# Kernel tuning notes

Measured on AMD Instinct MI355X. Metric: run time of the kernel, lower is better.

The kernel has to match this reference:

```python
import jax, jax.numpy as jnp
import numpy as np

GRID = 4
N_NODES = GRID * GRID
HEADS = 4
HID = 64

def _grid_edges(g=GRID):
    edges = []
    for i in range(g):
        for j in range(g):
            n = i * g + j
            if j + 1 < g:
                edges += [[n, n + 1], [n + 1, n]]
            if i + 1 < g:
                edges += [[n, n + g], [n + g, n]]
    for n in range(g * g):  # PyG GATConv default add_self_loops=True
        edges.append([n, n])
    e = np.asarray(edges, dtype=np.int32).T
    return jnp.asarray(e[0]), jnp.asarray(e[1])  # src (j), dst (i)

SRC, DST = _grid_edges()


def _layernorm(x, g, b, eps=1e-5):
    m = x.mean(-1, keepdims=True)
    v = ((x - m) ** 2).mean(-1, keepdims=True)
    return (x - m) * jax.lax.rsqrt(v + eps) * g + b


def _gat_conv(x, W, a_src, a_dst, bias, concat):
    # x: (B,N,Cin); W: (Cin,H*F); a_src,a_dst: (H,F)
    B, N, _ = x.shape
    H, F = a_src.shape
    xp = (x @ W).reshape(B, N, H, F)
    es = jnp.einsum('bnhf,hf->bnh', xp, a_src)  # alpha_src per node
    ed = jnp.einsum('bnhf,hf->bnh', xp, a_dst)  # alpha_dst per node
    logits = jax.nn.leaky_relu(es[:, SRC] + ed[:, DST], 0.2)  # (B,E,H)
    lt = logits.transpose(1, 0, 2)  # (E,B,H) for segment ops over edges
    mx = jax.ops.segment_max(lt, DST, num_segments=N)
    w = jnp.exp(lt - mx[DST])
    denom = jax.ops.segment_sum(w, DST, num_segments=N)
    alpha = w / denom[DST]  # softmax over incoming edges per dst node
    msg = alpha[..., None] * xp[:, SRC].transpose(1, 0, 2, 3)  # (E,B,H,F)
    out = jax.ops.segment_sum(msg, DST, num_segments=N).transpose(1, 0, 2, 3)  # (B,N,H,F)
    out = out.reshape(B, N, H * F) if concat else out.mean(axis=2)
    return out + bias


def _forward(x, in_w, in_b,
             gat0_w, gat0_asrc, gat0_adst, gat0_b,
             gat1_w, gat1_asrc, gat1_adst, gat1_b,
             gat2_w, gat2_asrc, gat2_adst, gat2_b,
             mlp_w1, mlp_b1, ln1_g, ln1_b,
             mlp_w2, mlp_b2, ln2_g, ln2_b):
    B = x.shape[0]
    # grid->graph: (B,C,H,W) -> (B, N, C)
    nodes = x.transpose(0, 2, 3, 1).reshape(B, N_NODES, -1)
    h = jax.nn.relu(nodes @ in_w + in_b)
    h = _gat_conv(h, gat0_w, gat0_asrc, gat0_adst, gat0_b, concat=True)
    h = jax.nn.relu(h)  # dropout is eval-mode identity
    h = _gat_conv(h, gat1_w, gat1_asrc, gat1_adst, gat1_b, concat=True)
    h = jax.nn.relu(h)
    h = _gat_conv(h, gat2_w, gat2_asrc, gat2_adst, gat2_b, concat=False)
    g = h.mean(axis=1)  # global_mean_pool over the fixed 16-node graph
    y = jax.nn.relu(_layernorm(g @ mlp_w1 + mlp_b1, ln1_g, ln1_b))
    out = jax.nn.relu(_layernorm(y @ mlp_w2 + mlp_b2, ln2_g, ln2_b))
    return out


def setup_inputs() -> dict:
    key = jax.random.key(0)
    ks = jax.random.split(key, 32)
    B, CIN, H, F = 4096, 16, HEADS, HID
    s = 0.1
    d = {
        'x': jax.random.normal(ks[0], (B, CIN, GRID, GRID), jnp.float32),
        'in_w': jax.random.normal(ks[1], (CIN, F)) * s,
        'in_b': jnp.zeros((F,)),
        'gat0_w': jax.random.normal(ks[2], (F, H * F)) * s,
        'gat0_asrc': jax.random.normal(ks[3], (H, F)) * s,
        'gat0_adst': jax.random.normal(ks[4], (H, F)) * s,
        'gat0_b': jnp.zeros((H * F,)),
        'gat1_w': jax.random.normal(ks[5], (H * F, H * F)) * s,
        'gat1_asrc': jax.random.normal(ks[6], (H, F)) * s,
        'gat1_adst': jax.random.normal(ks[7], (H, F)) * s,
        'gat1_b': jnp.zeros((H * F,)),
        'gat2_w': jax.random.normal(ks[8], (H * F, H * F)) * s,
        'gat2_asrc': jax.random.normal(ks[9], (H, F)) * s,
        'gat2_adst': jax.random.normal(ks[10], (H, F)) * s,
        'gat2_b': jnp.zeros((F,)),
        'mlp_w1': jax.random.normal(ks[11], (F, 128)) * s,
        'mlp_b1': jnp.zeros((128,)),
        'ln1_g': jnp.ones((128,)),
        'ln1_b': jnp.zeros((128,)),
        'mlp_w2': jax.random.normal(ks[12], (128, 256)) * s,
        'mlp_b2': jnp.zeros((256,)),
        'ln2_g': jnp.ones((256,)),
        'ln2_b': jnp.zeros((256,)),
    }
    return d


def reference(x, in_w, in_b,
              gat0_w, gat0_asrc, gat0_adst, gat0_b,
              gat1_w, gat1_asrc, gat1_adst, gat1_b,
              gat2_w, gat2_asrc, gat2_adst, gat2_b,
              mlp_w1, mlp_b1, ln1_g, ln1_b,
              mlp_w2, mlp_b2, ln2_g, ln2_b):
    return _forward(x, in_w, in_b,
                    gat0_w, gat0_asrc, gat0_adst, gat0_b,
                    gat1_w, gat1_asrc, gat1_adst, gat1_b,
                    gat2_w, gat2_asrc, gat2_adst, gat2_b,
                    mlp_w1, mlp_b1, ln1_g, ln1_b,
                    mlp_w2, mlp_b2, ln2_g, ln2_b)
```

## Files before the change

kernel.cpp:

```cpp
#include <hip/hip_runtime.h>
#include <math.h>

#define TPB 256
typedef short bfrag __attribute__((ext_vector_type(8)));
typedef float facc4 __attribute__((ext_vector_type(4)));
typedef unsigned int u32;

#define O_INW 0
#define O_G0  2048
#define O_G1  19456
#define O_G2  89088
#define O_W1  158720
#define O_W2  166912

__device__ __forceinline__ short f2bf(float x) {
    u32 u = __float_as_uint(x);
    u32 r = (u + 0x7fffu + ((u >> 16) & 1u)) >> 16;
    return (short)r;
}
__device__ __forceinline__ u32 pk2bf(float lo, float hi) {
    return ((u32)(unsigned short)f2bf(hi) << 16) | (u32)(unsigned short)f2bf(lo);
}

__device__ __forceinline__ int ht_sw(int row, int col) {
    return row * 256 + (col ^ ((row & 7) << 3));
}

__device__ __forceinline__ void pack_frag(const float* __restrict__ W, short* __restrict__ out,
                                          int blk, int NCOL, int TSTR) {
    int u = blk * 256 + threadIdx.x;
    int NT = NCOL >> 4;
    int j = u & 7, l = (u >> 3) & 63, q = u >> 9;
    int nt = q % NT, s = q / NT;
    int k = 32 * s + 8 * (l >> 4) + j;
    int c = 16 * nt + (l & 15);
    out[((s * TSTR + nt) * 64 + l) * 8 + j] = f2bf(W[k * NCOL + c]);
}

__device__ __forceinline__ void pack_fold(const float* __restrict__ W,
                                          const float* __restrict__ as_, const float* __restrict__ ad_,
                                          short* __restrict__ out, int blk, int TSTR) {
    int u = blk * 256 + threadIdx.x;
    int j = u & 7, l = (u >> 3) & 63, s = u >> 9;
    int c = l & 15;
    int k = 32 * s + 8 * (l >> 4) + j;
    float v = 0.f;
    if (c < 8) {
        int h = c >> 1;
        const float* a = (c & 1) ? ad_ : as_;
        for (int f = 0; f < 64; ++f) v += W[k * 256 + h * 64 + f] * a[h * 64 + f];
    }
    out[((s * TSTR + 16) * 64 + l) * 8 + j] = f2bf(v);
}

__device__ __forceinline__ void pack_inw(const float* __restrict__ inw, short* __restrict__ out, int blk) {
    int u = blk * 256 + threadIdx.x;
    int j = u & 7, l = (u >> 3) & 63, nt = u >> 9;
    int k = 8 * (l >> 4) + j;
    out[u] = (k < 16) ? f2bf(inw[k * 64 + 16 * nt + (l & 15)]) : (short)0;
}

__global__ void prep_all(const float* __restrict__ g0w, const float* __restrict__ g1w,
                         const float* __restrict__ g2w, const float* __restrict__ mw1,
                         const float* __restrict__ mw2, const float* __restrict__ inw,
                         const float* __restrict__ g0as, const float* __restrict__ g0ad,
                         const float* __restrict__ g1as, const float* __restrict__ g1ad,
                         const float* __restrict__ g2as, const float* __restrict__ g2ad,
                         short* __restrict__ ws) {
    int blk = blockIdx.x;
    if      (blk < 64)  pack_frag(g0w, ws + O_G0, blk,        256, 17);
    else if (blk < 320) pack_frag(g1w, ws + O_G1, blk - 64,   256, 17);
    else if (blk < 576) pack_frag(g2w, ws + O_G2, blk - 320,  256, 17);
    else if (blk < 608) pack_frag(mw1, ws + O_W1, blk - 576,  128, 8);
    else if (blk < 736) pack_frag(mw2, ws + O_W2, blk - 608,  256, 16);
    else if (blk < 744) pack_inw(inw, ws + O_INW, blk - 736);
    else if (blk < 748) pack_fold(g0w, g0as, g0ad, ws + O_G0, blk - 744, 17);
    else if (blk < 764) pack_fold(g1w, g1as, g1ad, ws + O_G1, blk - 748, 17);
    else                pack_fold(g2w, g2as, g2ad, ws + O_G2, blk - 764, 17);
}

template<int KSTEPS>
__device__ __forceinline__ void gat_core(
    const short* s_htA, const short* s_htB, const short* __restrict__ Wp,
    short* s_alphaM, short* s_xpA, short* s_xpB,
    facc4 agg[2][4]) {

    const int t = threadIdx.x;
    const int w = t >> 6, lane = t & 63, g = lane >> 4, ci = lane & 15;
    const facc4 fz = {0.f, 0.f, 0.f, 0.f};
    const bfrag* Wf = (const bfrag*)Wp;

    facc4 acc[2][4] = {{fz, fz, fz, fz}, {fz, fz, fz, fz}};
    facc4 acce = fz;
#pragma unroll 2
    for (int s = 0; s < KSTEPS; ++s) {
        bfrag a0 = *(const bfrag*)(s_htA + ht_sw(ci, s * 32 + g * 8));
        bfrag a1 = *(const bfrag*)(s_htB + ht_sw(ci, s * 32 + g * 8));
#pragma unroll
        for (int tt = 0; tt < 4; ++tt) {
            bfrag bf = Wf[(s * 17 + 4 * w + tt) * 64 + lane];
            acc[0][tt] = __builtin_amdgcn_mfma_f32_16x16x32_bf16(a0, bf, acc[0][tt], 0, 0, 0);
            acc[1][tt] = __builtin_amdgcn_mfma_f32_16x16x32_bf16(a1, bf, acc[1][tt], 0, 0, 0);
        }
        if (w < 2) {
            bfrag bfold = Wf[(s * 17 + 16) * 64 + lane];
            acce = __builtin_amdgcn_mfma_f32_16x16x32_bf16(w == 0 ? a0 : a1, bfold, acce, 0, 0, 0);
        }
    }

#pragma unroll
    for (int tt = 0; tt < 4; ++tt) {
        int col = 64 * w + 16 * tt + ci;
        *(uint2*)(s_xpA + col * 16 + 4 * g) =
            make_uint2(pk2bf(acc[0][tt][0], acc[0][tt][1]), pk2bf(acc[0][tt][2], acc[0][tt][3]));
        *(uint2*)(s_xpB + col * 16 + 4 * g) =
            make_uint2(pk2bf(acc[1][tt][0], acc[1][tt][1]), pk2bf(acc[1][tt][2], acc[1][tt][3]));
    }
    if (w < 2 && ci < 8) {
        int h = ci >> 1, isD = ci & 1;
#pragma unroll
        for (int r = 0; r < 4; ++r) {
            int idx = (4 * g + r) * 4 + h;
            float* padf = (float*)(s_alphaM + idx * 40 + 32);
            padf[w * 2 + isD] = acce[r];
        }
    }
    __syncthreads();

    if (t < 128) {
        int gr = t >> 6, tl = t & 63, d = tl & 15, h = tl >> 4;
        int ii = d >> 2, jj = d & 3;
        const int go = gr * 2;
        float edv = ((const float*)(s_alphaM + (d * 4 + h) * 40 + 32))[go + 1];
        bool v1 = (jj > 0), v2 = (jj < 3), v3 = (ii > 0), v4 = (ii < 3);
        int s1 = v1 ? d - 1 : d, s2 = v2 ? d + 1 : d;
        int s3 = v3 ? d - 4 : d, s4 = v4 ? d + 4 : d;
        float e0 = ((const float*)(s_alphaM + (d  * 4 + h) * 40 + 32))[go];
        float e1 = ((const float*)(s_alphaM + (s1 * 4 + h) * 40 + 32))[go];
        float e2 = ((const float*)(s_alphaM + (s2 * 4 + h) * 40 + 32))[go];
        float e3 = ((const float*)(s_alphaM + (s3 * 4 + h) * 40 + 32))[go];
        float e4 = ((const float*)(s_alphaM + (s4 * 4 + h) * 40 + 32))[go];
        float l0 = e0 + edv; l0 = (l0 > 0.f) ? l0 : 0.2f * l0;
        float l1 = e1 + edv; l1 = (l1 > 0.f) ? l1 : 0.2f * l1; l1 = v1 ? l1 : -1e30f;
        float l2 = e2 + edv; l2 = (l2 > 0.f) ? l2 : 0.2f * l2; l2 = v2 ? l2 : -1e30f;
        float l3 = e3 + edv; l3 = (l3 > 0.f) ? l3 : 0.2f * l3; l3 = v3 ? l3 : -1e30f;
        float l4 = e4 + edv; l4 = (l4 > 0.f) ? l4 : 0.2f * l4; l4 = v4 ? l4 : -1e30f;
        float mx = fmaxf(fmaxf(fmaxf(l0, l1), fmaxf(l2, l3)), l4);
        float w0 = __expf(l0 - mx), w1 = __expf(l1 - mx), w2 = __expf(l2 - mx);
        float w3 = __expf(l3 - mx), w4 = __expf(l4 - mx);
        float inv = 1.f / (w0 + w1 + w2 + w3 + w4);
        short* base = s_alphaM + (h * 16 + d) * 40 + gr * 16;
        base[s1] = f2bf(w1 * inv);
        base[s2] = f2bf(w2 * inv);
        base[s3] = f2bf(w3 * inv);
        base[s4] = f2bf(w4 * inv);
        base[d]  = f2bf(w0 * inv);
    }
    __syncthreads();

    bfrag araw = *(const bfrag*)(s_alphaM + (w * 16 + ci) * 40 + g * 8);
    const bfrag zf = {};
    bfrag af0 = (g < 2) ? araw : zf;
    bfrag af1 = (g < 2) ? zf : araw;
    const short* xsrc = (g < 2) ? s_xpA : s_xpB;
    const int xoff = (g & 1) * 8;
#pragma unroll
    for (int tt = 0; tt < 4; ++tt) {
        int col = 64 * w + 16 * tt + ci;
        bfrag xf = *(const bfrag*)(xsrc + col * 16 + xoff);
        agg[0][tt] = __builtin_amdgcn_mfma_f32_16x16x32_bf16(af0, xf, fz, 0, 0, 0);
        agg[1][tt] = __builtin_amdgcn_mfma_f32_16x16x32_bf16(af1, xf, fz, 0, 0, 0);
    }
}

__global__ __launch_bounds__(TPB, 4) void gat_fused(
    const float* __restrict__ x,  const float* __restrict__ in_b,
    const short* __restrict__ ws,
    const float* __restrict__ g0_b, const float* __restrict__ g1_b, const float* __restrict__ g2_b,
    const float* __restrict__ b1,   const float* __restrict__ ln1g, const float* __restrict__ ln1b,
    const float* __restrict__ b2,   const float* __restrict__ ln2g, const float* __restrict__ ln2b,
    float* __restrict__ out) {

    __shared__ __align__(16) short s_ht[2][16 * 256];
    __shared__ __align__(16) short s_xpA[256 * 16];
    __shared__ __align__(16) short s_xpB[256 * 16];
    __shared__ __align__(16) short s_alphaM[64 * 40];

    float* s_hsum = (float*)s_ht;
    short* s_gb   = (short*)((char*)s_ht + 2048);
    short* s_y2b  = (short*)((char*)s_ht + 2304);
    float* s_part = (float*)((char*)s_ht + 2816);

    const int b = blockIdx.x, t = threadIdx.x;
    const int w = t >> 6, lane = t & 63, g = lane >> 4, ci = lane & 15;
    const facc4 fz = {0.f, 0.f, 0.f, 0.f};

    {
        int row = t >> 2, q = t & 3;
        *(uint4*)(s_alphaM + row * 40 + q * 8) = make_uint4(0, 0, 0, 0);
    }

    {
        bfrag a0 = {}, a1 = {};
        if (g < 2) {
            float xv0[8], xv1[8];
#pragma unroll
            for (int j = 0; j < 8; ++j) {
                xv0[j] = x[(2 * b)     * 256 + (8 * g + j) * 16 + ci];
                xv1[j] = x[(2 * b + 1) * 256 + (8 * g + j) * 16 + ci];
            }
            u32* ap0 = (u32*)&a0; u32* ap1 = (u32*)&a1;
#pragma unroll
            for (int j = 0; j < 4; ++j) {
                ap0[j] = pk2bf(xv0[2 * j], xv0[2 * j + 1]);
                ap1[j] = pk2bf(xv1[2 * j], xv1[2 * j + 1]);
            }
        }
        bfrag bw = ((const bfrag*)(ws + O_INW))[w * 64 + lane];
        facc4 h0 = __builtin_amdgcn_mfma_f32_16x16x32_bf16(a0, bw, fz, 0, 0, 0);
        facc4 h1 = __builtin_amdgcn_mfma_f32_16x16x32_bf16(a1, bw, fz, 0, 0, 0);
        float ib = in_b[16 * w + ci];
#pragma unroll
        for (int r = 0; r < 4; ++r) {
            s_ht[0][ht_sw(4 * g + r, 16 * w + ci)] = f2bf(fmaxf(h0[r] + ib, 0.f));
            s_ht[1][ht_sw(4 * g + r, 16 * w + ci)] = f2bf(fmaxf(h1[r] + ib, 0.f));
        }
    }
    __syncthreads();

    facc4 agg[2][4];

    gat_core<2>(s_ht[0], s_ht[1], ws + O_G0, s_alphaM, s_xpA, s_xpB, agg);
#pragma unroll
    for (int tt = 0; tt < 4; ++tt) {
        float bb = g0_b[64 * w + 16 * tt + ci];
#pragma unroll
        for (int gr = 0; gr < 2; ++gr)
#pragma unroll
            for (int r = 0; r < 4; ++r)
                s_ht[gr][ht_sw(4 * g + r, 64 * w + 16 * tt + ci)] = f2bf(fmaxf(agg[gr][tt][r] + bb, 0.f));
    }
    __syncthreads();

    gat_core<8>(s_ht[0], s_ht[1], ws + O_G1, s_alphaM, s_xpA, s_xpB, agg);
#pragma unroll
    for (int tt = 0; tt < 4; ++tt) {
        float bb = g1_b[64 * w + 16 * tt + ci];
#pragma unroll
        for (int gr = 0; gr < 2; ++gr)
#pragma unroll
            for (int r = 0; r < 4; ++r)
                s_ht[gr][ht_sw(4 * g + r, 64 * w + 16 * tt + ci)] = f2bf(fmaxf(agg[gr][tt][r] + bb, 0.f));
    }
    __syncthreads();

    gat_core<8>(s_ht[0], s_ht[1], ws + O_G2, s_alphaM, s_xpA, s_xpB, agg);
#pragma unroll
    for (int gr = 0; gr < 2; ++gr)
#pragma unroll
        for (int tt = 0; tt < 4; ++tt) {
            float c = agg[gr][tt][0] + agg[gr][tt][1] + agg[gr][tt][2] + agg[gr][tt][3];
            c += __shfl_xor(c, 16);
            c += __shfl_xor(c, 32);
            if (lane < 16) s_hsum[gr * 256 + w * 64 + 16 * tt + lane] = c;
        }
    __syncthreads();
    if (t < 128) {
        int gr = t >> 6, f = t & 63;
        const float* hs = s_hsum + gr * 256;
        s_gb[gr * 64 + f] = f2bf(g2_b[f] + (hs[f] + hs[64 + f] + hs[128 + f] + hs[192 + f]) * (1.f / 64.f));
    }
    __syncthreads();

    float v1[2][2];
    {
        const bfrag* W1f = (const bfrag*)(ws + O_W1);
        facc4 m0 = fz, m1 = fz;
#pragma unroll
        for (int s = 0; s < 2; ++s) {
            bfrag a = {};
            if (ci < 2) a = *(const bfrag*)(s_gb + ci * 64 + 32 * s + 8 * g);
            m0 = __builtin_amdgcn_mfma_f32_16x16x32_bf16(a, W1f[(s * 8 + 2 * w + 0) * 64 + lane], m0, 0, 0, 0);
            m1 = __builtin_amdgcn_mfma_f32_16x16x32_bf16(a, W1f[(s * 8 + 2 * w + 1) * 64 + lane], m1, 0, 0, 0);
        }
        float bb0 = b1[32 * w + ci], bb1 = b1[32 * w + 16 + ci];
        v1[0][0] = m0[0] + bb0; v1[1][0] = m0[1] + bb0;
        v1[0][1] = m1[0] + bb1; v1[1][1] = m1[1] + bb1;
    }
    {
#pragma unroll
        for (int gr = 0; gr < 2; ++gr) {
            float u = v1[gr][0] + v1[gr][1];
            float q = v1[gr][0] * v1[gr][0] + v1[gr][1] * v1[gr][1];
            u += __shfl_xor(u, 1); u += __shfl_xor(u, 2); u += __shfl_xor(u, 4); u += __shfl_xor(u, 8);
            q += __shfl_xor(q, 1); q += __shfl_xor(q, 2); q += __shfl_xor(q, 4); q += __shfl_xor(q, 8);
            if (lane == 0) { s_part[gr * 8 + w] = u; s_part[gr * 8 + 4 + w] = q; }
        }
    }
    __syncthreads();
#pragma unroll
    for (int gr = 0; gr < 2; ++gr) {
        float sum = s_part[gr * 8 + 0] + s_part[gr * 8 + 1] + s_part[gr * 8 + 2] + s_part[gr * 8 + 3];
        float sq  = s_part[gr * 8 + 4] + s_part[gr * 8 + 5] + s_part[gr * 8 + 6] + s_part[gr * 8 + 7];
        float mn = sum * (1.f / 128.f);
        float var = sq * (1.f / 128.f) - mn * mn;
        float rs = rsqrtf(var + 1e-5f);
        if (g == 0) {
#pragma unroll
            for (int tt = 0; tt < 2; ++tt) {
                int col = 32 * w + 16 * tt + ci;
                s_y2b[gr * 128 + col] = f2bf(fmaxf((v1[gr][tt] - mn) * rs * ln1g[col] + ln1b[col], 0.f));
            }
        }
    }
    __syncthreads();

    float v2[2][4];
    {
        const bfrag* W2f = (const bfrag*)(ws + O_W2);
        facc4 m[4] = {fz, fz, fz, fz};
#pragma unroll 2
        for (int s = 0; s < 4; ++s) {
            bfrag a = {};
            if (ci < 2) a = *(const bfrag*)(s_y2b + ci * 128 + 32 * s + 8 * g);
#pragma unroll
            for (int tt = 0; tt < 4; ++tt)
                m[tt] = __builtin_amdgcn_mfma_f32_16x16x32_bf16(a, W2f[(s * 16 + 4 * w + tt) * 64 + lane], m[tt], 0, 0, 0);
        }
#pragma unroll
        for (int tt = 0; tt < 4; ++tt) {
            float bb = b2[64 * w + 16 * tt + ci];
            v2[0][tt] = m[tt][0] + bb;
            v2[1][tt] = m[tt][1] + bb;
        }
    }
    {
#pragma unroll
        for (int gr = 0; gr < 2; ++gr) {
            float u = v2[gr][0] + v2[gr][1] + v2[gr][2] + v2[gr][3];
            float q = v2[gr][0] * v2[gr][0] + v2[gr][1] * v2[gr][1] + v2[gr][2] * v2[gr][2] + v2[gr][3] * v2[gr][3];
            u += __shfl_xor(u, 1); u += __shfl_xor(u, 2); u += __shfl_xor(u, 4); u += __shfl_xor(u, 8);
            q += __shfl_xor(q, 1); q += __shfl_xor(q, 2); q += __shfl_xor(q, 4); q += __shfl_xor(q, 8);
            if (lane == 0) { s_part[gr * 8 + w] = u; s_part[gr * 8 + 4 + w] = q; }
        }
    }
    __syncthreads();
#pragma unroll
    for (int gr = 0; gr < 2; ++gr) {
        float sum = s_part[gr * 8 + 0] + s_part[gr * 8 + 1] + s_part[gr * 8 + 2] + s_part[gr * 8 + 3];
        float sq  = s_part[gr * 8 + 4] + s_part[gr * 8 + 5] + s_part[gr * 8 + 6] + s_part[gr * 8 + 7];
        float mn = sum * (1.f / 256.f);
        float var = sq * (1.f / 256.f) - mn * mn;
        float rs = rsqrtf(var + 1e-5f);
        if (g == 0) {
#pragma unroll
            for (int tt = 0; tt < 4; ++tt) {
                int col = 64 * w + 16 * tt + ci;
                out[(2 * b + gr) * 256 + col] = fmaxf((v2[gr][tt] - mn) * rs * ln2g[col] + ln2b[col], 0.f);
            }
        }
    }
}

extern "C" void kernel_launch(void* const* d_in, const int* in_sizes, int n_in,
                              void* d_out, int out_size, void* d_ws, size_t ws_size,
                              hipStream_t stream) {
    const float* x    = (const float*)d_in[0];
    const float* in_w = (const float*)d_in[1];
    const float* in_b = (const float*)d_in[2];
    const float* g0w  = (const float*)d_in[3];
    const float* g0as = (const float*)d_in[4];
    const float* g0ad = (const float*)d_in[5];
    const float* g0b  = (const float*)d_in[6];
    const float* g1w  = (const float*)d_in[7];
    const float* g1as = (const float*)d_in[8];
    const float* g1ad = (const float*)d_in[9];
    const float* g1b  = (const float*)d_in[10];
    const float* g2w  = (const float*)d_in[11];
    const float* g2as = (const float*)d_in[12];
    const float* g2ad = (const float*)d_in[13];
    const float* g2b  = (const float*)d_in[14];
    const float* w1   = (const float*)d_in[15];
    const float* b1   = (const float*)d_in[16];
    const float* ln1g = (const float*)d_in[17];
    const float* ln1b = (const float*)d_in[18];
    const float* w2   = (const float*)d_in[19];
    const float* b2   = (const float*)d_in[20];
    const float* ln2g = (const float*)d_in[21];
    const float* ln2b = (const float*)d_in[22];

    const int B = in_sizes[0] / 256;
    short* wsb = (short*)d_ws;

    prep_all<<<780, 256, 0, stream>>>(g0w, g1w, g2w, w1, w2, in_w,
                                      g0as, g0ad, g1as, g1ad, g2as, g2ad, wsb);

    gat_fused<<<B / 2, TPB, 0, stream>>>(
        x, in_b, wsb,
        g0b, g1b, g2b,
        b1, ln1g, ln1b,
        b2, ln2g, ln2b,
        (float*)d_out);
}
```

Baseline: 64.82 us.

## Double block size to 512 threads and split output columns across eight waves

Raises threads per block from 256 to 512, so eight wavefronts each compute 32 output columns of the GAT projections, aggregation and MLP layers instead of four waves computing 64. The input projection is split so each wave handles one graph and one 16-column tile. The LayerNorm partial-sum reductions are widened to eight waves. The aim is to cut per-block latency in a small-grid kernel by spreading the MFMA and LDS work over more waves, at the cost of more barrier participants and lower per-wave register reuse of the A fragments.

```diff
diff --git a/kernel.cpp b/kernel.cpp
--- a/kernel.cpp
+++ b/kernel.cpp
@@ -1,7 +1,7 @@
 #include <hip/hip_runtime.h>
 #include <math.h>
 
-#define TPB 256
+#define TPB 512
 typedef short bfrag __attribute__((ext_vector_type(8)));
 typedef float facc4 __attribute__((ext_vector_type(4)));
 typedef unsigned int u32;
@@ -83,22 +83,22 @@
 __device__ __forceinline__ void gat_core(
     const short* s_htA, const short* s_htB, const short* __restrict__ Wp,
     short* s_alphaM, short* s_xpA, short* s_xpB,
-    facc4 agg[2][4]) {
+    facc4 agg[2][2]) {
 
     const int t = threadIdx.x;
     const int w = t >> 6, lane = t & 63, g = lane >> 4, ci = lane & 15;
     const facc4 fz = {0.f, 0.f, 0.f, 0.f};
     const bfrag* Wf = (const bfrag*)Wp;
 
-    facc4 acc[2][4] = {{fz, fz, fz, fz}, {fz, fz, fz, fz}};
+    facc4 acc[2][2] = {{fz, fz}, {fz, fz}};
     facc4 acce = fz;
 #pragma unroll 2
     for (int s = 0; s < KSTEPS; ++s) {
         bfrag a0 = *(const bfrag*)(s_htA + ht_sw(ci, s * 32 + g * 8));
         bfrag a1 = *(const bfrag*)(s_htB + ht_sw(ci, s * 32 + g * 8));
 #pragma unroll
-        for (int tt = 0; tt < 4; ++tt) {
-            bfrag bf = Wf[(s * 17 + 4 * w + tt) * 64 + lane];
+        for (int tt = 0; tt < 2; ++tt) {
+            bfrag bf = Wf[(s * 17 + 2 * w + tt) * 64 + lane];
             acc[0][tt] = __builtin_amdgcn_mfma_f32_16x16x32_bf16(a0, bf, acc[0][tt], 0, 0, 0);
             acc[1][tt] = __builtin_amdgcn_mfma_f32_16x16x32_bf16(a1, bf, acc[1][tt], 0, 0, 0);
         }
@@ -109,8 +109,8 @@
     }
 
 #pragma unroll
-    for (int tt = 0; tt < 4; ++tt) {
-        int col = 64 * w + 16 * tt + ci;
+    for (int tt = 0; tt < 2; ++tt) {
+        int col = 32 * w + 16 * tt + ci;
         *(uint2*)(s_xpA + col * 16 + 4 * g) =
             make_uint2(pk2bf(acc[0][tt][0], acc[0][tt][1]), pk2bf(acc[0][tt][2], acc[0][tt][3]));
         *(uint2*)(s_xpB + col * 16 + 4 * g) =
@@ -158,22 +158,22 @@
     }
     __syncthreads();
 
-    bfrag araw = *(const bfrag*)(s_alphaM + (w * 16 + ci) * 40 + g * 8);
+    bfrag araw = *(const bfrag*)(s_alphaM + ((w >> 1) * 16 + ci) * 40 + g * 8);
     const bfrag zf = {};
     bfrag af0 = (g < 2) ? araw : zf;
     bfrag af1 = (g < 2) ? zf : araw;
     const short* xsrc = (g < 2) ? s_xpA : s_xpB;
     const int xoff = (g & 1) * 8;
 #pragma unroll
-    for (int tt = 0; tt < 4; ++tt) {
-        int col = 64 * w + 16 * tt + ci;
+    for (int tt = 0; tt < 2; ++tt) {
+        int col = 32 * w + 16 * tt + ci;
         bfrag xf = *(const bfrag*)(xsrc + col * 16 + xoff);
         agg[0][tt] = __builtin_amdgcn_mfma_f32_16x16x32_bf16(af0, xf, fz, 0, 0, 0);
         agg[1][tt] = __builtin_amdgcn_mfma_f32_16x16x32_bf16(af1, xf, fz, 0, 0, 0);
     }
 }
 
-__global__ __launch_bounds__(TPB, 4) void gat_fused(
+__global__ __launch_bounds__(TPB, 8) void gat_fused(
     const float* __restrict__ x,  const float* __restrict__ in_b,
     const short* __restrict__ ws,
     const float* __restrict__ g0_b, const float* __restrict__ g1_b, const float* __restrict__ g2_b,
@@ -195,62 +195,54 @@
     const int w = t >> 6, lane = t & 63, g = lane >> 4, ci = lane & 15;
     const facc4 fz = {0.f, 0.f, 0.f, 0.f};
 
-    {
+    if (t < 256) {
         int row = t >> 2, q = t & 3;
         *(uint4*)(s_alphaM + row * 40 + q * 8) = make_uint4(0, 0, 0, 0);
     }
 
     {
-        bfrag a0 = {}, a1 = {};
+        const int gi = w >> 2, nt = w & 3;
+        bfrag a0 = {};
         if (g < 2) {
-            float xv0[8], xv1[8];
-#pragma unroll
-            for (int j = 0; j < 8; ++j) {
-                xv0[j] = x[(2 * b)     * 256 + (8 * g + j) * 16 + ci];
-                xv1[j] = x[(2 * b + 1) * 256 + (8 * g + j) * 16 + ci];
-            }
-            u32* ap0 = (u32*)&a0; u32* ap1 = (u32*)&a1;
-#pragma unroll
-            for (int j = 0; j < 4; ++j) {
-                ap0[j] = pk2bf(xv0[2 * j], xv0[2 * j + 1]);
-                ap1[j] = pk2bf(xv1[2 * j], xv1[2 * j + 1]);
-            }
-        }
-        bfrag bw = ((const bfrag*)(ws + O_INW))[w * 64 + lane];
-        facc4 h0 = __builtin_amdgcn_mfma_f32_16x16x32_bf16(a0, bw, fz, 0, 0, 0);
-        facc4 h1 = __builtin_amdgcn_mfma_f32_16x16x32_bf16(a1, bw, fz, 0, 0, 0);
-        float ib = in_b[16 * w + ci];
-#pragma unroll
-        for (int r = 0; r < 4; ++r) {
-            s_ht[0][ht_sw(4 * g + r, 16 * w + ci)] = f2bf(fmaxf(h0[r] + ib, 0.f));
-            s_ht[1][ht_sw(4 * g + r, 16 * w + ci)] = f2bf(fmaxf(h1[r] + ib, 0.f));
-        }
-    }
-    __syncthreads();
-
-    facc4 agg[2][4];
+            float xv[8];
+#pragma unroll
+            for (int j = 0; j < 8; ++j) xv[j] = x[(2 * b + gi) * 256 + (8 * g + j) * 16 + ci];
+            u32* ap = (u32*)&a0;
+#pragma unroll
+            for (int j = 0; j < 4; ++j) ap[j] = pk2bf(xv[2 * j], xv[2 * j + 1]);
+        }
+        bfrag bw = ((const bfrag*)(ws + O_INW))[nt * 64 + lane];
+        facc4 h = __builtin_amdgcn_mfma_f32_16x16x32_bf16(a0, bw, fz, 0, 0, 0);
+        float ib = in_b[16 * nt + ci];
+#pragma unroll
+        for (int r = 0; r < 4; ++r)
+            s_ht[gi][ht_sw(4 * g + r, 16 * nt + ci)] = f2bf(fmaxf(h[r] + ib, 0.f));
+    }
+    __syncthreads();
+
+    facc4 agg[2][2];
 
     gat_core<2>(s_ht[0], s_ht[1], ws + O_G0, s_alphaM, s_xpA, s_xpB, agg);
 #pragma unroll
-    for (int tt = 0; tt < 4; ++tt) {
-        float bb = g0_b[64 * w + 16 * tt + ci];
+    for (int tt = 0; tt < 2; ++tt) {
+        float bb = g0_b[32 * w + 16 * tt + ci];
 #pragma unroll
         for (int gr = 0; gr < 2; ++gr)
 #pragma unroll
             for (int r = 0; r < 4; ++r)
-                s_ht[gr][ht_sw(4 * g + r, 64 * w + 16 * tt + ci)] = f2bf(fmaxf(agg[gr][tt][r] + bb, 0.f));
+                s_ht[gr][ht_sw(4 * g + r, 32 * w + 16 * tt + ci)] = f2bf(fmaxf(agg[gr][tt][r] + bb, 0.f));
     }
     __syncthreads();
 
     gat_core<8>(s_ht[0], s_ht[1], ws + O_G1, s_alphaM, s_xpA, s_xpB, agg);
 #pragma unroll
-    for (int tt = 0; tt < 4; ++tt) {
-        float bb = g1_b[64 * w + 16 * tt + ci];
+    for (int tt = 0; tt < 2; ++tt) {
+        float bb = g1_b[32 * w + 16 * tt + ci];
 #pragma unroll
         for (int gr = 0; gr < 2; ++gr)
 #pragma unroll
             for (int r = 0; r < 4; ++r)
-                s_ht[gr][ht_sw(4 * g + r, 64 * w + 16 * tt + ci)] = f2bf(fmaxf(agg[gr][tt][r] + bb, 0.f));
+                s_ht[gr][ht_sw(4 * g + r, 32 * w + 16 * tt + ci)] = f2bf(fmaxf(agg[gr][tt][r] + bb, 0.f));
     }
     __syncthreads();
 
@@ -258,11 +250,11 @@
 #pragma unroll
     for (int gr = 0; gr < 2; ++gr)
 #pragma unroll
-        for (int tt = 0; tt < 4; ++tt) {
+        for (int tt = 0; tt < 2; ++tt) {
             float c = agg[gr][tt][0] + agg[gr][tt][1] + agg[gr][tt][2] + agg[gr][tt][3];
             c += __shfl_xor(c, 16);
             c += __shfl_xor(c, 32);
-            if (lane < 16) s_hsum[gr * 256 + w * 64 + 16 * tt + lane] = c;
+            if (lane < 16) s_hsum[gr * 256 + 32 * w + 16 * tt + lane] = c;
         }
     __syncthreads();
     if (t < 128) {
@@ -272,90 +264,84 @@
     }
     __syncthreads();
 
-    float v1[2][2];
+    float v1[2];
     {
         const bfrag* W1f = (const bfrag*)(ws + O_W1);
-        facc4 m0 = fz, m1 = fz;
+        facc4 m0 = fz;
 #pragma unroll
         for (int s = 0; s < 2; ++s) {
             bfrag a = {};
             if (ci < 2) a = *(const bfrag*)(s_gb + ci * 64 + 32 * s + 8 * g);
-            m0 = __builtin_amdgcn_mfma_f32_16x16x32_bf16(a, W1f[(s * 8 + 2 * w + 0) * 64 + lane], m0, 0, 0, 0);
-            m1 = __builtin_amdgcn_mfma_f32_16x16x32_bf16(a, W1f[(s * 8 + 2 * w + 1) * 64 + lane], m1, 0, 0, 0);
-        }
-        float bb0 = b1[32 * w + ci], bb1 = b1[32 * w + 16 + ci];
-        v1[0][0] = m0[0] + bb0; v1[1][0] = m0[1] + bb0;
-        v1[0][1] = m1[0] + bb1; v1[1][1] = m1[1] + bb1;
-    }
-    {
-#pragma unroll
-        for (int gr = 0; gr < 2; ++gr) {
-            float u = v1[gr][0] + v1[gr][1];
-            float q = v1[gr][0] * v1[gr][0] + v1[gr][1] * v1[gr][1];
-            u += __shfl_xor(u, 1); u += __shfl_xor(u, 2); u += __shfl_xor(u, 4); u += __shfl_xor(u, 8);
-            q += __shfl_xor(q, 1); q += __shfl_xor(q, 2); q += __shfl_xor(q, 4); q += __shfl_xor(q, 8);
-            if (lane == 0) { s_part[gr * 8 + w] = u; s_part[gr * 8 + 4 + w] = q; }
-        }
-    }
-    __syncthreads();
+            m0 = __builtin_amdgcn_mfma_f32_16x16x32_bf16(a, W1f[(s * 8 + w) * 64 + lane], m0, 0, 0, 0);
+        }
+        float bb = b1[16 * w + ci];
+        v1[0] = m0[0] + bb;
+        v1[1] = m0[1] + bb;
+    }
 #pragma unroll
     for (int gr = 0; gr < 2; ++gr) {
-        float sum = s_part[gr * 8 + 0] + s_part[gr * 8 + 1] + s_part[gr * 8 + 2] + s_part[gr * 8 + 3];
-        float sq  = s_part[gr * 8 + 4] + s_part[gr * 8 + 5] + s_part[gr * 8 + 6] + s_part[gr * 8 + 7];
+        float u = (g == 0) ? v1[gr] : 0.f;
+        float q = (g == 0) ? v1[gr] * v1[gr] : 0.f;
+        u += __shfl_xor(u, 1); u += __shfl_xor(u, 2); u += __shfl_xor(u, 4); u += __shfl_xor(u, 8);
+        q += __shfl_xor(q, 1); q += __shfl_xor(q, 2); q += __shfl_xor(q, 4); q += __shfl_xor(q, 8);
+        if (lane == 0) { s_part[gr * 16 + w] = u; s_part[gr * 16 + 8 + w] = q; }
+    }
+    __syncthreads();
+#pragma unroll
+    for (int gr = 0; gr < 2; ++gr) {
+        const float* sp = s_part + gr * 16;
+        float sum = sp[0] + sp[1] + sp[2] + sp[3] + sp[4] + sp[5] + sp[6] + sp[7];
+        float sq  = sp[8] + sp[9] + sp[10] + sp[11] + sp[12] + sp[13] + sp[14] + sp[15];
         float mn = sum * (1.f / 128.f);
         float var = sq * (1.f / 128.f) - mn * mn;
         float rs = rsqrtf(var + 1e-5f);
         if (g == 0) {
-#pragma unroll
-            for (int tt = 0; tt < 2; ++tt) {
-                int col = 32 * w + 16 * tt + ci;
-                s_y2b[gr * 128 + col] = f2bf(fmaxf((v1[gr][tt] - mn) * rs * ln1g[col] + ln1b[col], 0.f));
-            }
-        }
-    }
-    __syncthreads();
-
-    float v2[2][4];
+            int col = 16 * w + ci;
+            s_y2b[gr * 128 + col] = f2bf(fmaxf((v1[gr] - mn) * rs * ln1g[col] + ln1b[col], 0.f));
+        }
+    }
+    __syncthreads();
+
+    float v2[2][2];
     {
         const bfrag* W2f = (const bfrag*)(ws + O_W2);
-        facc4 m[4] = {fz, fz, fz, fz};
+        facc4 m[2] = {fz, fz};
 #pragma unroll 2
         for (int s = 0; s < 4; ++s) {
             bfrag a = {};
             if (ci < 2) a = *(const bfrag*)(s_y2b + ci * 128 + 32 * s + 8 * g);
 #pragma unroll
-            for (int tt = 0; tt < 4; ++tt)
-                m[tt] = __builtin_amdgcn_mfma_f32_16x16x32_bf16(a, W2f[(s * 16 + 4 * w + tt) * 64 + lane], m[tt], 0, 0, 0);
-        }
-#pragma unroll
-        for (int tt = 0; tt < 4; ++tt) {
-            float bb = b2[64 * w + 16 * tt + ci];
+            for (int tt = 0; tt < 2; ++tt)
+                m[tt] = __builtin_amdgcn_mfma_f32_16x16x32_bf16(a, W2f[(s * 16 + 2 * w + tt) * 64 + lane], m[tt], 0, 0, 0);
+        }
+#pragma unroll
+        for (int tt = 0; tt < 2; ++tt) {
+            float bb = b2[32 * w + 16 * tt + ci];
             v2[0][tt] = m[tt][0] + bb;
             v2[1][tt] = m[tt][1] + bb;
         }
     }
-    {
-#pragma unroll
-        for (int gr = 0; gr < 2; ++gr) {
-            float u = v2[gr][0] + v2[gr][1] + v2[gr][2] + v2[gr][3];
-            float q = v2[gr][0] * v2[gr][0] + v2[gr][1] * v2[gr][1] + v2[gr][2] * v2[gr][2] + v2[gr][3] * v2[gr][3];
-            u += __shfl_xor(u, 1); u += __shfl_xor(u, 2); u += __shfl_xor(u, 4); u += __shfl_xor(u, 8);
-            q += __shfl_xor(q, 1); q += __shfl_xor(q, 2); q += __shfl_xor(q, 4); q += __shfl_xor(q, 8);
-            if (lane == 0) { s_part[gr * 8 + w] = u; s_part[gr * 8 + 4 + w] = q; }
-        }
-    }
-    __syncthreads();
 #pragma unroll
     for (int gr = 0; gr < 2; ++gr) {
-        float sum = s_part[gr * 8 + 0] + s_part[gr * 8 + 1] + s_part[gr * 8 + 2] + s_part[gr * 8 + 3];
-        float sq  = s_part[gr * 8 + 4] + s_part[gr * 8 + 5] + s_part[gr * 8 + 6] + s_part[gr * 8 + 7];
+        float u = (g == 0) ? v2[gr][0] + v2[gr][1] : 0.f;
+        float q = (g == 0) ? v2[gr][0] * v2[gr][0] + v2[gr][1] * v2[gr][1] : 0.f;
+        u += __shfl_xor(u, 1); u += __shfl_xor(u, 2); u += __shfl_xor(u, 4); u += __shfl_xor(u, 8);
+        q += __shfl_xor(q, 1); q += __shfl_xor(q, 2); q += __shfl_xor(q, 4); q += __shfl_xor(q, 8);
+        if (lane == 0) { s_part[gr * 16 + w] = u; s_part[gr * 16 + 8 + w] = q; }
+    }
+    __syncthreads();
+#pragma unroll
+    for (int gr = 0; gr < 2; ++gr) {
+        const float* sp = s_part + gr * 16;
+        float sum = sp[0] + sp[1] + sp[2] + sp[3] + sp[4] + sp[5] + sp[6] + sp[7];
+        float sq  = sp[8] + sp[9] + sp[10] + sp[11] + sp[12] + sp[13] + sp[14] + sp[15];
         float mn = sum * (1.f / 256.f);
         float var = sq * (1.f / 256.f) - mn * mn;
         float rs = rsqrtf(var + 1e-5f);
         if (g == 0) {
 #pragma unroll
-            for (int tt = 0; tt < 4; ++tt) {
-                int col = 64 * w + 16 * tt + ci;
+            for (int tt = 0; tt < 2; ++tt) {
+                int col = 32 * w + 16 * tt + ci;
                 out[(2 * b + gr) * 256 + col] = fmaxf((v2[gr][tt] - mn) * rs * ln2g[col] + ln2b[col], 0.f);
             }
         }
```

Result: slower. 79.18 us (+22.1%).

## Share one xp LDS buffer across both batch groups to cut shared memory

Applied to the files above, without the earlier changes.

Replaces the two per-group projected-feature LDS buffers with a single shared buffer. The second group's projection is written only after the first group's aggregation MFMAs have consumed the buffer, with extra barriers between the phases, and the bias+ReLU writeback is folded into gat_core. This lowers LDS per block, which may let more blocks reside per CU, at the cost of two extra __syncthreads per GAT layer and some serialisation of the aggregation.

```diff
diff --git a/kernel.cpp b/kernel.cpp
--- a/kernel.cpp
+++ b/kernel.cpp
@@ -79,23 +79,24 @@
     else                pack_fold(g2w, g2as, g2ad, ws + O_G2, blk - 764, 17);
 }
 
-template<int KSTEPS>
+template<int KSTEPS, bool WRITE_HT>
 __device__ __forceinline__ void gat_core(
-    const short* s_htA, const short* s_htB, const short* __restrict__ Wp,
-    short* s_alphaM, short* s_xpA, short* s_xpB,
+    short* s_ht0, short* s_ht1, const short* __restrict__ Wp,
+    short* s_alphaM, short* s_xp, const float* __restrict__ bias,
     facc4 agg[2][4]) {
 
     const int t = threadIdx.x;
     const int w = t >> 6, lane = t & 63, g = lane >> 4, ci = lane & 15;
     const facc4 fz = {0.f, 0.f, 0.f, 0.f};
+    const bfrag zf = {};
     const bfrag* Wf = (const bfrag*)Wp;
 
     facc4 acc[2][4] = {{fz, fz, fz, fz}, {fz, fz, fz, fz}};
     facc4 acce = fz;
 #pragma unroll 2
     for (int s = 0; s < KSTEPS; ++s) {
-        bfrag a0 = *(const bfrag*)(s_htA + ht_sw(ci, s * 32 + g * 8));
-        bfrag a1 = *(const bfrag*)(s_htB + ht_sw(ci, s * 32 + g * 8));
+        bfrag a0 = *(const bfrag*)(s_ht0 + ht_sw(ci, s * 32 + g * 8));
+        bfrag a1 = *(const bfrag*)(s_ht1 + ht_sw(ci, s * 32 + g * 8));
 #pragma unroll
         for (int tt = 0; tt < 4; ++tt) {
             bfrag bf = Wf[(s * 17 + 4 * w + tt) * 64 + lane];
@@ -111,10 +112,8 @@
 #pragma unroll
     for (int tt = 0; tt < 4; ++tt) {
         int col = 64 * w + 16 * tt + ci;
-        *(uint2*)(s_xpA + col * 16 + 4 * g) =
+        *(uint2*)(s_xp + col * 16 + 4 * g) =
             make_uint2(pk2bf(acc[0][tt][0], acc[0][tt][1]), pk2bf(acc[0][tt][2], acc[0][tt][3]));
-        *(uint2*)(s_xpB + col * 16 + 4 * g) =
-            make_uint2(pk2bf(acc[1][tt][0], acc[1][tt][1]), pk2bf(acc[1][tt][2], acc[1][tt][3]));
     }
     if (w < 2 && ci < 8) {
         int h = ci >> 1, isD = ci & 1;
@@ -159,17 +158,57 @@
     __syncthreads();
 
     bfrag araw = *(const bfrag*)(s_alphaM + (w * 16 + ci) * 40 + g * 8);
-    const bfrag zf = {};
-    bfrag af0 = (g < 2) ? araw : zf;
-    bfrag af1 = (g < 2) ? zf : araw;
-    const short* xsrc = (g < 2) ? s_xpA : s_xpB;
     const int xoff = (g & 1) * 8;
+
+    {
+        bfrag af0 = (g < 2) ? araw : zf;
+#pragma unroll
+        for (int tt = 0; tt < 4; ++tt) {
+            int col = 64 * w + 16 * tt + ci;
+            bfrag xf = zf;
+            if (g < 2) xf = *(const bfrag*)(s_xp + col * 16 + xoff);
+            agg[0][tt] = __builtin_amdgcn_mfma_f32_16x16x32_bf16(af0, xf, fz, 0, 0, 0);
+        }
+    }
+    __syncthreads();
+
 #pragma unroll
     for (int tt = 0; tt < 4; ++tt) {
         int col = 64 * w + 16 * tt + ci;
-        bfrag xf = *(const bfrag*)(xsrc + col * 16 + xoff);
-        agg[0][tt] = __builtin_amdgcn_mfma_f32_16x16x32_bf16(af0, xf, fz, 0, 0, 0);
-        agg[1][tt] = __builtin_amdgcn_mfma_f32_16x16x32_bf16(af1, xf, fz, 0, 0, 0);
+        *(uint2*)(s_xp + col * 16 + 4 * g) =
+            make_uint2(pk2bf(acc[1][tt][0], acc[1][tt][1]), pk2bf(acc[1][tt][2], acc[1][tt][3]));
+    }
+    if (WRITE_HT) {
+#pragma unroll
+        for (int tt = 0; tt < 4; ++tt) {
+            int col = 64 * w + 16 * tt + ci;
+            float bb = bias[col];
+#pragma unroll
+            for (int r = 0; r < 4; ++r)
+                s_ht0[ht_sw(4 * g + r, col)] = f2bf(fmaxf(agg[0][tt][r] + bb, 0.f));
+        }
+    }
+    __syncthreads();
+
+    {
+        bfrag af1 = (g < 2) ? zf : araw;
+#pragma unroll
+        for (int tt = 0; tt < 4; ++tt) {
+            int col = 64 * w + 16 * tt + ci;
+            bfrag xf = zf;
+            if (g >= 2) xf = *(const bfrag*)(s_xp + col * 16 + xoff);
+            agg[1][tt] = __builtin_amdgcn_mfma_f32_16x16x32_bf16(af1, xf, fz, 0, 0, 0);
+        }
+    }
+    if (WRITE_HT) {
+#pragma unroll
+        for (int tt = 0; tt < 4; ++tt) {
+            int col = 64 * w + 16 * tt + ci;
+            float bb = bias[col];
+#pragma unroll
+            for (int r = 0; r < 4; ++r)
+                s_ht1[ht_sw(4 * g + r, col)] = f2bf(fmaxf(agg[1][tt][r] + bb, 0.f));
+        }
     }
 }
 
@@ -182,8 +221,7 @@
     float* __restrict__ out) {
 
     __shared__ __align__(16) short s_ht[2][16 * 256];
-    __shared__ __align__(16) short s_xpA[256 * 16];
-    __shared__ __align__(16) short s_xpB[256 * 16];
+    __shared__ __align__(16) short s_xp[256 * 16];
     __shared__ __align__(16) short s_alphaM[64 * 40];
 
     float* s_hsum = (float*)s_ht;
@@ -230,31 +268,13 @@
 
     facc4 agg[2][4];
 
-    gat_core<2>(s_ht[0], s_ht[1], ws + O_G0, s_alphaM, s_xpA, s_xpB, agg);
-#pragma unroll
-    for (int tt = 0; tt < 4; ++tt) {
-        float bb = g0_b[64 * w + 16 * tt + ci];
-#pragma unroll
-        for (int gr = 0; gr < 2; ++gr)
-#pragma unroll
-            for (int r = 0; r < 4; ++r)
-                s_ht[gr][ht_sw(4 * g + r, 64 * w + 16 * tt + ci)] = f2bf(fmaxf(agg[gr][tt][r] + bb, 0.f));
-    }
-    __syncthreads();
-
-    gat_core<8>(s_ht[0], s_ht[1], ws + O_G1, s_alphaM, s_xpA, s_xpB, agg);
-#pragma unroll
-    for (int tt = 0; tt < 4; ++tt) {
-        float bb = g1_b[64 * w + 16 * tt + ci];
-#pragma unroll
-        for (int gr = 0; gr < 2; ++gr)
-#pragma unroll
-            for (int r = 0; r < 4; ++r)
-                s_ht[gr][ht_sw(4 * g + r, 64 * w + 16 * tt + ci)] = f2bf(fmaxf(agg[gr][tt][r] + bb, 0.f));
-    }
-    __syncthreads();
-
-    gat_core<8>(s_ht[0], s_ht[1], ws + O_G2, s_alphaM, s_xpA, s_xpB, agg);
+    gat_core<2, true>(s_ht[0], s_ht[1], ws + O_G0, s_alphaM, s_xp, g0_b, agg);
+    __syncthreads();
+
+    gat_core<8, true>(s_ht[0], s_ht[1], ws + O_G1, s_alphaM, s_xp, g1_b, agg);
+    __syncthreads();
+
+    gat_core<8, false>(s_ht[0], s_ht[1], ws + O_G2, s_alphaM, s_xp, g2_b, agg);
 #pragma unroll
     for (int gr = 0; gr < 2; ++gr)
 #pragma unroll
```

Result: slower. 67.56 us (+4.2%).
